# Optimization experiments

Hardware: AMD Instinct MI355X
Metric: run time of the kernel (lower is better)

Reference implementation:

```python
import jax, jax.numpy as jnp
import numpy as np

B, T, C, H, HS = 2, 2048, 1024, 16, 64
W_SIZE = 128
BLK = 64
NB = T // BLK            # 32 blocks
NSEL = 8                 # selected blocks per (b, h)
EPS = 1e-8


def setup_inputs() -> dict:
    key = jax.random.key(0)
    ks = jax.random.split(key, 12)
    s = 0.02
    return {
        "hidden_states": jax.random.normal(ks[0], (B, T, C), dtype=jnp.float32),
        "Wq": jax.random.normal(ks[1], (C, C), dtype=jnp.float32) * s,
        "bq": jnp.zeros((C,), jnp.float32),
        "Wk": jax.random.normal(ks[2], (C, C), dtype=jnp.float32) * s,
        "bk": jnp.zeros((C,), jnp.float32),
        "Wv": jax.random.normal(ks[3], (C, C), dtype=jnp.float32) * s,
        "bv": jnp.zeros((C,), jnp.float32),
        "Wo": jax.random.normal(ks[4], (C, C), dtype=jnp.float32) * s,
        "bo": jnp.zeros((C,), jnp.float32),
        "Wg": jax.random.normal(ks[5], (C, 3), dtype=jnp.float32) * s,
        "bg": jnp.zeros((3,), jnp.float32),
    }


def _sdpa(q, k, v, mask):
    # q: [B,H,Tq,HS], k/v: [B,H,S,HS], mask: [Tq,S] bool (True = attend)
    scale = 1.0 / jnp.sqrt(jnp.asarray(HS, q.dtype))
    scores = jnp.einsum('bhqd,bhkd->bhqk', q, k) * scale
    scores = jnp.where(mask, scores, jnp.asarray(-jnp.inf, scores.dtype))
    return jnp.einsum('bhqk,bhkd->bhqd', jax.nn.softmax(scores, axis=-1), v)


def _forward(x, Wq, bq, Wk, bk, Wv, bv, Wo, bo, Wg, bg):
    q = (x @ Wq + bq).reshape(B, T, H, HS).transpose(0, 2, 1, 3)
    k = (x @ Wk + bk).reshape(B, T, H, HS).transpose(0, 2, 1, 3)
    v = (x @ Wv + bv).reshape(B, T, H, HS).transpose(0, 2, 1, 3)

    gates = jax.nn.softmax(x @ Wg + bg, axis=-1)  # [B,T,3]
    g_sl, g_sel, g_cmp = gates[..., 0:1], gates[..., 1:2], gates[..., 2:3]

    i = jnp.arange(T)[:, None]

    # --- sliding-window branch (causal AND within window band) ---
    j = jnp.arange(T)[None, :]
    slide_mask = (j <= i) & (i - j <= W_SIZE)
    out_sl = _sdpa(q, k, v, slide_mask)

    # --- block representatives (mean-pooled K/V blocks) ---
    kb = k.reshape(B, H, NB, BLK, HS)
    vb = v.reshape(B, H, NB, BLK, HS)
    k_rep = kb.mean(axis=3)  # [B,H,NB,HS]

    # cosine similarity of each query vs each block rep, averaged over T
    qn = q / jnp.maximum(jnp.linalg.norm(q, axis=-1, keepdims=True), EPS)
    kn = k_rep / jnp.maximum(jnp.linalg.norm(k_rep, axis=-1, keepdims=True), EPS)
    global_scores = jnp.einsum('bhtd,bhnd->bhtn', qn, kn).mean(axis=2)  # [B,H,NB]
    _, top_idx = jax.lax.top_k(global_scores, NSEL)  # [B,H,NSEL]

    # gather selected K/V blocks
    sel_k = jnp.take_along_axis(kb, top_idx[..., None, None], axis=2).reshape(B, H, NSEL * BLK, HS)
    sel_v = jnp.take_along_axis(vb, top_idx[..., None, None], axis=2).reshape(B, H, NSEL * BLK, HS)

    # torch is_causal with Tq != S is top-left aligned: allow j <= i
    js = jnp.arange(NSEL * BLK)[None, :]
    out_sel = _sdpa(q, sel_k, sel_v, js <= i)

    # --- compressed branch over block reps ---
    v_cmp = vb.mean(axis=3)  # [B,H,NB,HS]
    jc = jnp.arange(NB)[None, :]
    out_cmp = _sdpa(q, k_rep, v_cmp, jc <= i)

    def merge(o):
        return o.transpose(0, 2, 1, 3).reshape(B, T, C)

    out = g_sl * merge(out_sl) + g_sel * merge(out_sel) + g_cmp * merge(out_cmp)
    return out @ Wo + bo


def reference(hidden_states, Wq, bq, Wk, bk, Wv, bv, Wo, bo, Wg, bg):
    return _forward(hidden_states, Wq, bq, Wk, bk, Wv, bv, Wo, bo, Wg, bg)
```

## Files before the change

kernel.cpp:

```cpp
#include <hip/hip_runtime.h>
#include <hip/hip_bf16.h>
#include <math.h>

#define Bc   2
#define Tc   2048
#define Cc   1024
#define Hc   16
#define HSc  64
#define WSZ  128
#define BLKc 64
#define NBc  32
#define NSELc 8
#define Mrows (Bc*Tc)
#define QCH  32
#define SOFT_C 4.0f

typedef __attribute__((ext_vector_type(8))) _Float16 half8;
typedef __attribute__((ext_vector_type(4))) float f32x4v;
typedef __attribute__((ext_vector_type(8))) unsigned short ushort8v;

__device__ __forceinline__ float wave_sum(float v) {
    #pragma unroll
    for (int o = 32; o; o >>= 1) v += __shfl_xor(v, o);
    return v;
}

__device__ __forceinline__ unsigned short f2h(float f) {
    _Float16 h = (_Float16)f;
    unsigned short u;
    __builtin_memcpy(&u, &h, 2);
    return u;
}
__device__ __forceinline__ float h2f(unsigned short u) {
    _Float16 h;
    __builtin_memcpy(&h, &u, 2);
    return (float)h;
}

__device__ __forceinline__ void gload16(const void* g, void* l) {
    __builtin_amdgcn_global_load_lds(
        (const __attribute__((address_space(1))) void*)g,
        (__attribute__((address_space(3))) void*)l, 16, 0, 0);
}

__global__ __launch_bounds__(256)
void cvt_front_kernel(const float* __restrict__ x, unsigned short* __restrict__ xb,
                      const float* __restrict__ Wg, const float* __restrict__ bg,
                      float* __restrict__ gates,
                      const float* __restrict__ W0, const float* __restrict__ W1,
                      const float* __restrict__ W2, const float* __restrict__ W3,
                      unsigned short* __restrict__ D012, unsigned short* __restrict__ D3)
{
    __shared__ float tile[64][65];
    const int bx = blockIdx.x;
    if (bx < 4096) {
        int i = (bx * 256 + threadIdx.x) * 4;
        float4 v = *(const float4*)&x[i];
        ushort4 o;
        o.x = f2h(v.x); o.y = f2h(v.y); o.z = f2h(v.z); o.w = f2h(v.w);
        *(ushort4*)&xb[i] = o;
        return;
    }
    if (bx < 5120) {
        const int row  = (bx - 4096) * 4 + (threadIdx.x >> 6);
        const int lane = threadIdx.x & 63;
        const float* xr = x + (size_t)row * Cc;
        float p0 = 0, p1 = 0, p2 = 0;
        #pragma unroll
        for (int it = 0; it < 4; ++it) {
            int k4 = lane * 4 + it * 256;
            float4 xv = *(const float4*)&xr[k4];
            float4 w0 = *(const float4*)&Wg[k4 * 3];
            float4 w1 = *(const float4*)&Wg[k4 * 3 + 4];
            float4 w2 = *(const float4*)&Wg[k4 * 3 + 8];
            p0 += xv.x * w0.x + xv.y * w0.w + xv.z * w1.z + xv.w * w2.y;
            p1 += xv.x * w0.y + xv.y * w1.x + xv.z * w1.w + xv.w * w2.z;
            p2 += xv.x * w0.z + xv.y * w1.y + xv.z * w2.x + xv.w * w2.w;
        }
        p0 = wave_sum(p0); p1 = wave_sum(p1); p2 = wave_sum(p2);
        if (lane == 0) {
            p0 += bg[0]; p1 += bg[1]; p2 += bg[2];
            float m = fmaxf(p0, fmaxf(p1, p2));
            float e0 = expf(p0 - m), e1 = expf(p1 - m), e2 = expf(p2 - m);
            float s = e0 + e1 + e2;
            gates[row * 3 + 0] = e0 / s;
            gates[row * 3 + 1] = e1 / s;
            gates[row * 3 + 2] = e2 / s;
        }
        return;
    }
    const int lin = bx - 5120;
    const int z = lin >> 8;
    const int n0 = (lin & 15) * 64, k0 = ((lin >> 4) & 15) * 64;
    const float* W = (z == 0) ? W0 : (z == 1) ? W1 : (z == 2) ? W2 : W3;
    unsigned short* WT = (z < 3) ? (D012 + (size_t)z * 1024 * 1024) : D3;
    const int tid = threadIdx.x;
    #pragma unroll
    for (int it = 0; it < 16; ++it) {
        int l2 = tid + it * 256;
        int r = l2 >> 6, c = l2 & 63;
        tile[r][c] = W[(size_t)(k0 + r) * 1024 + n0 + c];
    }
    __syncthreads();
    #pragma unroll
    for (int it = 0; it < 16; ++it) {
        int l2 = tid + it * 256;
        int n = l2 >> 6, k = l2 & 63;
        WT[(size_t)(n0 + n) * 1024 + k0 + k] = f2h(tile[k][n]);
    }
}


#define FENCE asm volatile("" ::: "memory")
#define BAR() do { FENCE; __builtin_amdgcn_s_barrier(); FENCE; } while(0)
#define WAIT_LGKM0() do { asm volatile("s_waitcnt lgkmcnt(0)" ::: "memory"); \
                          __builtin_amdgcn_sched_barrier(0); } while(0)
#define WAIT_VM(N) do { asm volatile("s_waitcnt vmcnt(" #N ")" ::: "memory"); } while(0)

#define LDA(BUF, MH) do { \
    const unsigned short* _p = &lds[BUF][0][(wmo + (MH)*64 + r16) * 64]; \
    a0[0] = *(const half8*)(_p +        cc0); a1[0] = *(const half8*)(_p +        cc1); \
    a0[1] = *(const half8*)(_p + 1024 + cc0); a1[1] = *(const half8*)(_p + 1024 + cc1); \
    a0[2] = *(const half8*)(_p + 2048 + cc0); a1[2] = *(const half8*)(_p + 2048 + cc1); \
    a0[3] = *(const half8*)(_p + 3072 + cc0); a1[3] = *(const half8*)(_p + 3072 + cc1); \
} while(0)

#define LDB(BUF, NH) do { \
    const unsigned short* _p = &lds[BUF][1][(wno + (NH)*32 + r16) * 64]; \
    b0[0] = *(const half8*)(_p +        cc0); b1[0] = *(const half8*)(_p +        cc1); \
    b0[1] = *(const half8*)(_p + 1024 + cc0); b1[1] = *(const half8*)(_p + 1024 + cc1); \
} while(0)

#define CLP(I, J, MH, NH) \
    acc[(MH)*4+(I)][(NH)*2+(J)] = __builtin_amdgcn_mfma_f32_16x16x32_f16(a0[I], b0[J], acc[(MH)*4+(I)][(NH)*2+(J)], 0, 0, 0); \
    acc[(MH)*4+(I)][(NH)*2+(J)] = __builtin_amdgcn_mfma_f32_16x16x32_f16(a1[I], b1[J], acc[(MH)*4+(I)][(NH)*2+(J)], 0, 0, 0);
#define CL(MH, NH) do { \
    __builtin_amdgcn_s_setprio(1); \
    CLP(0,0,MH,NH) CLP(0,1,MH,NH) CLP(1,0,MH,NH) CLP(1,1,MH,NH) \
    CLP(2,0,MH,NH) CLP(2,1,MH,NH) CLP(3,0,MH,NH) CLP(3,1,MH,NH) \
    __builtin_amdgcn_s_setprio(0); \
} while(0)

#define STAGEA(BUF, G, TILE) do { \
    size_t _co = (size_t)(TILE) * 64 + scol_x; \
    gload16(Ag + (size_t)(m0 +       (G)*64 + wid*8 + l8) * 1024 + _co, \
            &lds[BUF][0][((G)*64 + wid*8) * 64]); \
    gload16(Ag + (size_t)(m0 + 128 + (G)*64 + wid*8 + l8) * 1024 + _co, \
            &lds[BUF][0][(128 + (G)*64 + wid*8) * 64]); \
} while(0)

#define STAGEB(BUF, G, TILE) do { \
    size_t _co = (size_t)(TILE) * 64 + scol_x; \
    int _r0 = (wid >> 2) * 64 + (G)*32 + (wid & 3) * 8; \
    gload16(BTg + (size_t)(n0 +       _r0 + l8) * 1024 + _co, \
            &lds[BUF][1][_r0 * 64]); \
    gload16(BTg + (size_t)(n0 + 128 + _r0 + l8) * 1024 + _co, \
            &lds[BUF][1][(128 + _r0) * 64]); \
} while(0)

__global__ __launch_bounds__(512, 2)
void mfma_gemm_qkv8(const unsigned short* __restrict__ Ag,
                    const unsigned short* __restrict__ BTg,
                    const float* __restrict__ bq, const float* __restrict__ bk,
                    const float* __restrict__ bv,
                    unsigned short* __restrict__ Qh, unsigned short* __restrict__ Kf,
                    unsigned short* __restrict__ Vf)
{
    __shared__ unsigned short lds[2][2][256 * 64];
    const int tid  = threadIdx.x;
    const int lane = tid & 63, wid = tid >> 6;
    const int quad = lane >> 4, r16 = lane & 15;
    const int m0 = blockIdx.y * 256, n0 = blockIdx.x * 256;
    const int wmo = (wid >> 2) * 128;
    const int wno = (wid & 3) * 64;
    const int l8 = lane >> 3;
    const int scol_x = ((lane & 7) ^ l8) * 8;
    const int xsw = (r16 & 7) * 8;
    const int cc0 = (quad * 8) ^ xsw;
    const int cc1 = (32 + quad * 8) ^ xsw;

    f32x4v acc[8][4];
    #pragma unroll
    for (int i = 0; i < 8; ++i)
        #pragma unroll
        for (int j = 0; j < 4; ++j)
            acc[i][j] = (f32x4v){0.f, 0.f, 0.f, 0.f};

    half8 a0[4], a1[4], b0[2], b1[2];

    STAGEA(0, 0, 0); STAGEB(0, 1, 0); STAGEA(0, 1, 0); STAGEB(0, 0, 0);
    STAGEA(1, 0, 1); STAGEB(1, 1, 1);
    WAIT_VM(4);
    BAR();

    for (int it = 0; it < 8; ++it) {
        const int t1 = 2 * it + 1, t2v = 2 * it + 2, t3v = 2 * it + 3;
        const bool s2 = (t2v < 16), s3 = (t3v < 16);
        LDA(0, 0); LDB(0, 0);
        STAGEA(1, 1, t1);
        BAR(); WAIT_LGKM0();
        CL(0, 0);
        BAR();
        LDB(0, 1);
        STAGEB(1, 0, t1);
        BAR(); WAIT_LGKM0();
        CL(0, 1);
        BAR();
        LDA(0, 1);
        if (s2) STAGEA(0, 0, t2v);
        BAR(); WAIT_LGKM0();
        CL(1, 1);
        BAR();
        LDB(0, 0);
        if (s2) STAGEB(0, 1, t2v);
        BAR(); WAIT_LGKM0();
        CL(1, 0);
        if (it == 7) { WAIT_VM(0); } else { WAIT_VM(4); }
        BAR();
        LDA(1, 0); LDB(1, 0);
        if (s2) STAGEA(0, 1, t2v);
        BAR(); WAIT_LGKM0();
        CL(0, 0);
        BAR();
        LDB(1, 1);
        if (s2) STAGEB(0, 0, t2v);
        BAR(); WAIT_LGKM0();
        CL(0, 1);
        BAR();
        LDA(1, 1);
        if (s3) STAGEA(1, 0, t3v);
        BAR(); WAIT_LGKM0();
        CL(1, 1);
        BAR();
        LDB(1, 0);
        if (s3) STAGEB(1, 1, t3v);
        BAR(); WAIT_LGKM0();
        CL(1, 0);
        if (it < 7) WAIT_VM(4);
        BAR();
    }

    const int which = n0 >> 10;
    const float* bias = (which == 0) ? bq : ((which == 1) ? bk : bv);
    unsigned short* dst = (which == 0) ? Qh : ((which == 1) ? Kf : Vf);
    const float sc = (which == 0) ? 0.125f : 1.0f;
    #pragma unroll
    for (int i = 0; i < 8; ++i) {
        int mbase = m0 + wmo + i * 16 + quad * 4;
        #pragma unroll
        for (int j = 0; j < 4; ++j) {
            int n = n0 + wno + j * 16 + r16;
            int nn = n & 1023;
            float bvv = bias[nn];
            int h = nn >> 6, d = nn & 63;
            #pragma unroll
            for (int r = 0; r < 4; ++r) {
                int m = mbase + r;
                int b = m >> 11, t = m & 2047;
                float v = (acc[i][j][r] + bvv) * sc;
                dst[(((size_t)(b * Hc + h) * Tc) + t) * HSc + d] = f2h(v);
            }
        }
    }
}

#define OSTAGE(BUF, TILE) do { \
    size_t _t = (size_t)(TILE) * 64 + scol; \
    gload16(A  + (size_t)(m0 +      wid*8 + l8) * 1024 + _t, &As[BUF][( 0 + wid*64)*8]); \
    gload16(A  + (size_t)(m0 + 32 + wid*8 + l8) * 1024 + _t, &As[BUF][(256 + wid*64)*8]); \
    gload16(BT + (size_t)(n0 +      wid*8 + l8) * 1024 + _t, &Bs[BUF][( 0 + wid*64)*8]); \
    gload16(BT + (size_t)(n0 + 32 + wid*8 + l8) * 1024 + _t, &Bs[BUF][(256 + wid*64)*8]); \
    gload16(BT + (size_t)(n0 + 64 + wid*8 + l8) * 1024 + _t, &Bs[BUF][(512 + wid*64)*8]); \
    gload16(BT + (size_t)(n0 + 96 + wid*8 + l8) * 1024 + _t, &Bs[BUF][(768 + wid*64)*8]); \
} while(0)

__global__ __launch_bounds__(256, 2)
void mfma_gemm_oproj(const unsigned short* __restrict__ A,
                     const unsigned short* __restrict__ BT,
                     const float* __restrict__ bias,
                     float* __restrict__ Y)
{
    __shared__ unsigned short As[3][64 * 64];
    __shared__ unsigned short Bs[3][128 * 64];
    const int tid  = threadIdx.x;
    const int lane = tid & 63;
    const int wid  = tid >> 6;
    const int quad = lane >> 4, r16 = lane & 15;
    const int m0 = blockIdx.y * 64, n0 = blockIdx.x * 128;
    const int wm = (wid >> 1) * 32, wn = (wid & 1) * 64;
    const int l8 = lane >> 3;
    const int scol = ((lane & 7) ^ l8) * 8;
    const int xsw = (r16 & 7) * 8;
    const int cc0 = (quad * 8) ^ xsw;
    const int cc1 = (32 + quad * 8) ^ xsw;

    f32x4v acc[2][4];
    #pragma unroll
    for (int i = 0; i < 2; ++i)
        #pragma unroll
        for (int j = 0; j < 4; ++j)
            acc[i][j] = (f32x4v){0.f, 0.f, 0.f, 0.f};

    OSTAGE(0, 0); OSTAGE(1, 1);
    WAIT_VM(6);
    BAR();

    for (int t = 0; t < 16; ++t) {
        const int cb = t % 3;
        if (t + 2 < 16) OSTAGE((t + 2) % 3, t + 2);
        half8 af[2][2], bf[4][2];
        #pragma unroll
        for (int i = 0; i < 2; ++i) {
            const unsigned short* p = &As[cb][(wm + i * 16 + r16) * 64];
            af[i][0] = *(const half8*)(p + cc0);
            af[i][1] = *(const half8*)(p + cc1);
        }
        #pragma unroll
        for (int j = 0; j < 4; ++j) {
            const unsigned short* p = &Bs[cb][(wn + j * 16 + r16) * 64];
            bf[j][0] = *(const half8*)(p + cc0);
            bf[j][1] = *(const half8*)(p + cc1);
        }
        __builtin_amdgcn_s_setprio(1);
        #pragma unroll
        for (int i = 0; i < 2; ++i)
            #pragma unroll
            for (int j = 0; j < 4; ++j) {
                acc[i][j] = __builtin_amdgcn_mfma_f32_16x16x32_f16(af[i][0], bf[j][0], acc[i][j], 0, 0, 0);
                acc[i][j] = __builtin_amdgcn_mfma_f32_16x16x32_f16(af[i][1], bf[j][1], acc[i][j], 0, 0, 0);
            }
        __builtin_amdgcn_s_setprio(0);
        if (t + 2 < 16) { WAIT_VM(6); } else { WAIT_VM(0); }
        BAR();
    }

    #pragma unroll
    for (int i = 0; i < 2; ++i) {
        int mbase = m0 + wm + i * 16 + quad * 4;
        #pragma unroll
        for (int j = 0; j < 4; ++j) {
            int n = n0 + wn + j * 16 + r16;
            float bv = bias[n];
            #pragma unroll
            for (int r = 0; r < 4; ++r)
                Y[(size_t)(mbase + r) * 1024 + n] = acc[i][j][r] + bv;
        }
    }
}

__global__ __launch_bounds__(256)
void vtrans_stats_kernel(const unsigned short* __restrict__ Kf,
                         const unsigned short* __restrict__ Vf,
                         const unsigned short* __restrict__ Qh,
                         unsigned short* __restrict__ Vt,
                         float* __restrict__ krep,
                         unsigned short* __restrict__ krep16,
                         unsigned short* __restrict__ vcmpT16,
                         float* __restrict__ qpart)
{
    __shared__ unsigned short vtile[64][65];
    __shared__ unsigned short ktile[64][65];
    __shared__ float rinv[64];
    const int nb = blockIdx.x, bh = blockIdx.y;
    const int t0 = nb * BLKc;
    const int tid = threadIdx.x;
    const int c4 = (tid & 15) * 4, r = tid >> 4;
    const unsigned short* vsrc = Vf + ((size_t)bh * Tc + t0) * HSc;
    const unsigned short* ksrc = Kf + ((size_t)bh * Tc + t0) * HSc;
    #pragma unroll
    for (int it = 0; it < 4; ++it) {
        int tt = r + it * 16;
        *(ushort4*)&vtile[tt][c4] = *(const ushort4*)&vsrc[(size_t)tt * HSc + c4];
        *(ushort4*)&ktile[tt][c4] = *(const ushort4*)&ksrc[(size_t)tt * HSc + c4];
    }
    __syncthreads();
    unsigned short* dst = Vt + (size_t)bh * HSc * Tc + t0;
    #pragma unroll
    for (int it = 0; it < 4; ++it) {
        int d = r + it * 16;
        ushort4 o;
        o.x = vtile[c4 + 0][d]; o.y = vtile[c4 + 1][d];
        o.z = vtile[c4 + 2][d]; o.w = vtile[c4 + 3][d];
        *(ushort4*)&dst[(size_t)d * Tc + c4] = o;
    }
    const int wid = tid >> 6, lane = tid & 63;
    if (wid == 0) {
        const int d = lane;
        float sk = 0.f, sv = 0.f;
        #pragma unroll 8
        for (int t = 0; t < BLKc; ++t) {
            sk += h2f(ktile[t][d]);
            sv += h2f(vtile[t][d]);
        }
        float km = sk * (1.0f / BLKc), vm = sv * (1.0f / BLKc);
        krep[((size_t)bh * NBc + nb) * HSc + d] = km;
        krep16[(size_t)bh * 4096 + nb * 64 + d] = f2h(km);
        krep16[(size_t)bh * 4096 + (nb + 32) * 64 + d] = 0;
        vcmpT16[(size_t)bh * 4096 + d * 64 + nb] = f2h(vm);
        vcmpT16[(size_t)bh * 4096 + d * 64 + nb + 32] = 0;
    } else if (wid == 1) {
        const unsigned short* qbase = Qh + ((size_t)bh * Tc + t0) * HSc;
        {
            const unsigned short* qr = qbase + (size_t)lane * HSc;
            float ss = 0.f;
            #pragma unroll
            for (int d8 = 0; d8 < 8; ++d8) {
                ushort8v v8 = *(const ushort8v*)&qr[d8 * 8];
                #pragma unroll
                for (int j = 0; j < 8; ++j) { float f = h2f(v8[j]); ss += f * f; }
            }
            rinv[lane] = 1.0f / fmaxf(sqrtf(ss), 1e-8f);
        }
        float acc = 0.f;
        #pragma unroll 8
        for (int t = 0; t < 64; ++t)
            acc += h2f(qbase[(size_t)t * HSc + lane]) * rinv[t];
        qpart[((size_t)bh * QCH + nb) * HSc + lane] = acc;
    }
}

__global__ __launch_bounds__(64)
void topk_kernel(const float* __restrict__ qpart, const float* __restrict__ krep,
                 int* __restrict__ topidx)
{
    int bh = blockIdx.x, lane = threadIdx.x;
    __shared__ float sc[NBc];
    __shared__ float qbs[HSc];
    float qa = 0.0f;
    #pragma unroll
    for (int c = 0; c < QCH; c++)
        qa += qpart[((size_t)bh * QCH + c) * HSc + lane];
    qbs[lane] = qa * (1.0f / Tc);
    __syncthreads();
    if (lane < NBc) {
        float dot = 0, nk = 0;
        for (int d = 0; d < HSc; d++) {
            float kv = krep[((size_t)bh * NBc + lane) * HSc + d];
            nk += kv * kv;
            dot += qbs[d] * kv;
        }
        sc[lane] = dot / fmaxf(sqrtf(nk), 1e-8f);
    }
    __syncthreads();
    if (lane == 0) {
        for (int s = 0; s < NSELc; s++) {
            int best = 0; float bv = sc[0];
            for (int n = 1; n < NBc; n++)
                if (sc[n] > bv) { bv = sc[n]; best = n; }
            topidx[bh * NSELc + s] = best;
            sc[best] = -INFINITY;
        }
    }
}

__device__ __forceinline__ void fa_desc(int i, int nslide, int nsel, int q0,
                                        const int* __restrict__ topidx, int bh,
                                        int& kb, int& p0v, int& wl, int& kl, int& bid)
{
    if (i < nslide)             { kb = q0 - (nslide - 1 - i) * 64;
                                  p0v = kb; wl = WSZ; kl = 64; bid = 0; }
    else if (i < nslide + nsel) { int s = i - nslide;
                                  kb = topidx[bh * NSELc + s] * BLKc;
                                  p0v = s * BLKc; wl = 1 << 30; kl = 64; bid = 1; }
    else                        { kb = 0; p0v = 0; wl = 1 << 30; kl = NBc; bid = 2; }
}

__device__ __forceinline__ void fa_ldtile(int kb, int bid,
                                          const unsigned short* __restrict__ kbh,
                                          const unsigned short* __restrict__ vbh,
                                          const unsigned short* __restrict__ krepb,
                                          const unsigned short* __restrict__ vcmpb,
                                          int r0, int seg,
                                          ushort8v& k0, ushort8v& k1,
                                          ushort8v& v0, ushort8v& v1)
{
    const unsigned short *kp, *vp;
    int vs;
    if (bid < 2) { kp = kbh + (size_t)kb * HSc; vp = vbh + kb; vs = Tc; }
    else         { kp = krepb; vp = vcmpb; vs = 64; }
    k0 = *(const ushort8v*)(kp + (size_t)r0 * HSc + seg * 8);
    k1 = *(const ushort8v*)(kp + (size_t)(r0 + 32) * HSc + seg * 8);
    v0 = *(const ushort8v*)(vp + (size_t)r0 * vs + seg * 8);
    v1 = *(const ushort8v*)(vp + (size_t)(r0 + 32) * vs + seg * 8);
}

__device__ __forceinline__ void fa_qkt(const unsigned short* __restrict__ Kh,
                                       half8 aq0, half8 aq1, int l16, int kc0, int kc1,
                                       f32x4v s[4])
{
    #pragma unroll
    for (int t = 0; t < 4; ++t) {
        f32x4v sa = (f32x4v){0.f, 0.f, 0.f, 0.f};
        half8 b0 = *(const half8*)&Kh[(t * 16 + l16) * 64 + kc0];
        half8 b1 = *(const half8*)&Kh[(t * 16 + l16) * 64 + kc1];
        sa = __builtin_amdgcn_mfma_f32_16x16x32_f16(aq0, b0, sa, 0, 0, 0);
        sa = __builtin_amdgcn_mfma_f32_16x16x32_f16(aq1, b1, sa, 0, 0, 0);
        s[t] = sa;
    }
}

__device__ __forceinline__ void fa_expph(const f32x4v s[4], int p0v, int wl, int kl,
                                         int qg0, int prow, int l16,
                                         unsigned short* __restrict__ Ph)
{
    #pragma unroll
    for (int t = 0; t < 4; ++t) {
        int kk = t * 16 + l16;
        bool kok = kk < kl;
        int jt = p0v + kk;
        #pragma unroll
        for (int r = 0; r < 4; ++r) {
            bool valid = kok && ((unsigned)(qg0 + r - jt) <= (unsigned)wl);
            float p = valid ? __expf(s[t][r] - SOFT_C) : 0.0f;
            int row = prow + r;
            Ph[row * 64 + (kk ^ ((row & 7) * 8))] = f2h(p);
        }
    }
}

__device__ __forceinline__ void fa_pv(const unsigned short* __restrict__ Vt,
                                      const unsigned short* __restrict__ Ph,
                                      half8 ones, int wq, int l16, int kc0, int kc1,
                                      f32x4v o[4], f32x4v& o5)
{
    const int prd = (wq + l16) * 64;
    half8 ap0 = *(const half8*)&Ph[prd + kc0];
    half8 ap1 = *(const half8*)&Ph[prd + kc1];
    o5 = __builtin_amdgcn_mfma_f32_16x16x32_f16(ap0, ones, o5, 0, 0, 0);
    o5 = __builtin_amdgcn_mfma_f32_16x16x32_f16(ap1, ones, o5, 0, 0, 0);
    #pragma unroll
    for (int dt = 0; dt < 4; ++dt) {
        half8 v0 = *(const half8*)&Vt[(dt * 16 + l16) * 64 + kc0];
        half8 v1 = *(const half8*)&Vt[(dt * 16 + l16) * 64 + kc1];
        o[dt] = __builtin_amdgcn_mfma_f32_16x16x32_f16(ap0, v0, o[dt], 0, 0, 0);
        o[dt] = __builtin_amdgcn_mfma_f32_16x16x32_f16(ap1, v1, o[dt], 0, 0, 0);
    }
}

__global__ __launch_bounds__(256, 2)
void fattn_kernel(const unsigned short* __restrict__ Qh16,
                  const unsigned short* __restrict__ Kf,
                  const unsigned short* __restrict__ Vtg,
                  const unsigned short* __restrict__ krep16,
                  const unsigned short* __restrict__ vcmpT16,
                  const int* __restrict__ topidx,
                  const float* __restrict__ gates, unsigned short* __restrict__ merged)
{
    __shared__ unsigned short KH[2][64 * 64];
    __shared__ unsigned short VT[2][64 * 64];
    __shared__ unsigned short Ph[64 * 64];

    const int qt = blockIdx.x;
    const int bh = blockIdx.y;
    const int b  = bh >> 4, h = bh & 15;
    const int tid  = threadIdx.x;
    const int wid  = tid >> 6, lane = tid & 63;
    const int l16  = lane & 15, quad = lane >> 4;
    const int q0 = qt * 64;
    const int wq = wid * 16;
    const int qg0 = q0 + wq + quad * 4;
    const int prow = wq + quad * 4;

    const int nslide = (qt < 2 ? qt : 2) + 1;
    const int nsel   = (qt + 1 < NSELc) ? (qt + 1) : NSELc;
    const int nt     = nslide + nsel + 1;

    half8 aq0, aq1, ones;
    {
        const unsigned short* qrow = Qh16 + ((size_t)bh * Tc + q0 + wq + l16) * HSc;
        aq0 = *(const half8*)(qrow + quad * 8);
        aq1 = *(const half8*)(qrow + 32 + quad * 8);
        #pragma unroll
        for (int j = 0; j < 8; ++j) ones[j] = (_Float16)1.0f;
    }

    f32x4v o[4], macc[4];
    f32x4v o5 = (f32x4v){0.f, 0.f, 0.f, 0.f};
    #pragma unroll
    for (int dt = 0; dt < 4; ++dt) {
        o[dt]    = (f32x4v){0.f, 0.f, 0.f, 0.f};
        macc[dt] = (f32x4v){0.f, 0.f, 0.f, 0.f};
    }

    const int seg = tid & 7, r0 = tid >> 3;
    const int stc = (seg ^ (r0 & 7)) * 8;
    const int st0 = r0 * 64 + stc;
    const int st1 = (r0 + 32) * 64 + stc;
    const int psw = (l16 & 7) * 8;
    const int kc0 = (quad * 8) ^ psw;
    const int kc1 = (32 + quad * 8) ^ psw;

    const unsigned short* kbh  = Kf  + (size_t)bh * Tc * HSc;
    const unsigned short* vbh  = Vtg + (size_t)bh * HSc * Tc;
    const unsigned short* krepb = krep16  + (size_t)bh * 4096;
    const unsigned short* vcmpb = vcmpT16 + (size_t)bh * 4096;

#define FA_MERGE(PB) do { \
    _Pragma("unroll") \
    for (int r = 0; r < 4; ++r) { \
        float g = gates[((size_t)b * Tc + qg0 + r) * 3 + (PB)]; \
        float inv = g / o5[r]; \
        _Pragma("unroll") \
        for (int dt = 0; dt < 4; ++dt) { macc[dt][r] += inv * o[dt][r]; o[dt][r] = 0.f; } \
        o5[r] = 0.f; \
    } \
} while(0)

    {
        int kb, p0v, wl, kl, bid;
        ushort8v k0, k1, v0, v1;
        fa_desc(0, nslide, nsel, q0, topidx, bh, kb, p0v, wl, kl, bid);
        fa_ldtile(kb, bid, kbh, vbh, krepb, vcmpb, r0, seg, k0, k1, v0, v1);
        *(ushort8v*)&KH[0][st0] = k0; *(ushort8v*)&KH[0][st1] = k1;
        *(ushort8v*)&VT[0][st0] = v0; *(ushort8v*)&VT[0][st1] = v1;
        fa_desc(1, nslide, nsel, q0, topidx, bh, kb, p0v, wl, kl, bid);
        fa_ldtile(kb, bid, kbh, vbh, krepb, vcmpb, r0, seg, k0, k1, v0, v1);
        *(ushort8v*)&KH[1][st0] = k0; *(ushort8v*)&KH[1][st1] = k1;
        *(ushort8v*)&VT[1][st0] = v0; *(ushort8v*)&VT[1][st1] = v1;
    }
    __syncthreads();

    int pb = 0;
    for (int i = 0; i < nt; i += 2) {
        const bool dual = (i + 1 < nt);
        const bool pf2  = (i + 2 < nt);
        const bool pf3  = (i + 3 < nt);

        ushort8v pk0[2], pk1[2], pv0[2], pv1[2];
        if (pf2) {
            int kb, p0v, wl, kl, bid;
            fa_desc(i + 2, nslide, nsel, q0, topidx, bh, kb, p0v, wl, kl, bid);
            fa_ldtile(kb, bid, kbh, vbh, krepb, vcmpb, r0, seg,
                      pk0[0], pk1[0], pv0[0], pv1[0]);
        }
        if (pf3) {
            int kb, p0v, wl, kl, bid;
            fa_desc(i + 3, nslide, nsel, q0, topidx, bh, kb, p0v, wl, kl, bid);
            fa_ldtile(kb, bid, kbh, vbh, krepb, vcmpb, r0, seg,
                      pk0[1], pk1[1], pv0[1], pv1[1]);
        }

        int kbA, p0A, wlA, klA, bidA;
        fa_desc(i, nslide, nsel, q0, topidx, bh, kbA, p0A, wlA, klA, bidA);
        int kbB, p0B, wlB, klB, bidB = bidA;
        if (dual) fa_desc(i + 1, nslide, nsel, q0, topidx, bh, kbB, p0B, wlB, klB, bidB);

        f32x4v sA[4], sB[4];
        fa_qkt(KH[0], aq0, aq1, l16, kc0, kc1, sA);
        if (dual) fa_qkt(KH[1], aq0, aq1, l16, kc0, kc1, sB);

        if (bidA != pb) { FA_MERGE(pb); pb = bidA; }
        fa_expph(sA, p0A, wlA, klA, qg0, prow, l16, Ph);
        fa_pv(VT[0], Ph, ones, wq, l16, kc0, kc1, o, o5);

        if (dual) {
            if (bidB != pb) { FA_MERGE(pb); pb = bidB; }
            fa_expph(sB, p0B, wlB, klB, qg0, prow, l16, Ph);
            fa_pv(VT[1], Ph, ones, wq, l16, kc0, kc1, o, o5);
        }

        if (pf2) {
            __syncthreads();
            *(ushort8v*)&KH[0][st0] = pk0[0]; *(ushort8v*)&KH[0][st1] = pk1[0];
            *(ushort8v*)&VT[0][st0] = pv0[0]; *(ushort8v*)&VT[0][st1] = pv1[0];
            if (pf3) {
                *(ushort8v*)&KH[1][st0] = pk0[1]; *(ushort8v*)&KH[1][st1] = pk1[1];
                *(ushort8v*)&VT[1][st0] = pv0[1]; *(ushort8v*)&VT[1][st1] = pv1[1];
            }
            __syncthreads();
        }
    }

    #pragma unroll
    for (int r = 0; r < 4; ++r) {
        float g = gates[((size_t)b * Tc + qg0 + r) * 3 + 2];
        float inv = g / o5[r];
        #pragma unroll
        for (int dt = 0; dt < 4; ++dt) macc[dt][r] += inv * o[dt][r];
    }

    #pragma unroll
    for (int r = 0; r < 4; ++r) {
        size_t mrow = (size_t)b * Tc + qg0 + r;
        #pragma unroll
        for (int dt = 0; dt < 4; ++dt)
            merged[mrow * Cc + h * HSc + dt * 16 + l16] = f2h(macc[dt][r]);
    }
#undef FA_MERGE
}

extern "C" void kernel_launch(void* const* d_in, const int* in_sizes, int n_in,
                              void* d_out, int out_size, void* d_ws, size_t ws_size,
                              hipStream_t stream)
{
    const float* x  = (const float*)d_in[0];
    const float* Wq = (const float*)d_in[1];
    const float* bq = (const float*)d_in[2];
    const float* Wk = (const float*)d_in[3];
    const float* bk = (const float*)d_in[4];
    const float* Wv = (const float*)d_in[5];
    const float* bv = (const float*)d_in[6];
    const float* Wo = (const float*)d_in[7];
    const float* bo = (const float*)d_in[8];
    const float* Wg = (const float*)d_in[9];
    const float* bg = (const float*)d_in[10];
    float* out = (float*)d_out;
    float* ws  = (float*)d_ws;

    unsigned short* Qh16 = (unsigned short*)(ws + 0);
    unsigned short* Kf16 = (unsigned short*)(ws + 2097152);
    unsigned short* Vf16 = (unsigned short*)(ws + 4194304);
    unsigned short* Vt16 = (unsigned short*)(ws + 6291456);
    unsigned short* Mgb  = (unsigned short*)(ws + 8388608);
    unsigned short* xb   = (unsigned short*)(ws + 10485760);
    unsigned short* WqkvT = (unsigned short*)(ws + 12582912);
    unsigned short* WoT   = (unsigned short*)(ws + 14155776);
    float* gates = ws + 14680064;
    float* krep  = ws + 14692352;
    unsigned short* krep16  = (unsigned short*)(ws + 14757888);
    unsigned short* vcmpT16 = (unsigned short*)(ws + 14823424);
    float* qpart = ws + 14888960;
    int*   topidx = (int*)(ws + 14954496);

    cvt_front_kernel<<<6144, 256, 0, stream>>>(x, xb, Wg, bg, gates,
                                               Wq, Wk, Wv, Wo, WqkvT, WoT);

    mfma_gemm_qkv8<<<dim3(12, 16), 512, 0, stream>>>(xb, WqkvT, bq, bk, bv,
                                                     Qh16, Kf16, Vf16);
    vtrans_stats_kernel<<<dim3(NBc, Bc * Hc), 256, 0, stream>>>(Kf16, Vf16, Qh16,
                                                                Vt16, krep, krep16,
                                                                vcmpT16, qpart);
    topk_kernel<<<Bc * Hc, 64, 0, stream>>>(qpart, krep, topidx);
    fattn_kernel<<<dim3(Tc / 64, Bc * Hc), 256, 0, stream>>>(Qh16, Kf16, Vt16,
                                                             krep16, vcmpT16,
                                                             topidx, gates, Mgb);
    mfma_gemm_oproj<<<dim3(8, 64), 256, 0, stream>>>(Mgb, WoT, bo, out);
}
```

Measured before the change: 201.4 us.

## Software-pipeline attention loop with 4-slot K/V ring and double-buffered P

Replaces the two-tiles-per-iteration loop with a one-tile-per-iteration software pipeline. The QK^T and exp of tile i now run alongside the PV product of tile i-1, using a 4-deep shared K/V ring buffer and double-buffered probability tiles. The aim is to cut barriers from two per tile pair to one per tile and to overlap MFMA work across stages. In exchange, shared memory per block roughly doubles, which could limit occupancy, and the merge ordering now depends on the deferred PV.

```diff
diff --git a/kernel.cpp b/kernel.cpp
--- a/kernel.cpp
+++ b/kernel.cpp
@@ -546,9 +546,9 @@
                   const int* __restrict__ topidx,
                   const float* __restrict__ gates, unsigned short* __restrict__ merged)
 {
-    __shared__ unsigned short KH[2][64 * 64];
-    __shared__ unsigned short VT[2][64 * 64];
-    __shared__ unsigned short Ph[64 * 64];
+    __shared__ unsigned short KH[4][64 * 64];
+    __shared__ unsigned short VT[4][64 * 64];
+    __shared__ unsigned short Ph[2][64 * 64];
 
     const int qt = blockIdx.x;
     const int bh = blockIdx.y;
@@ -620,57 +620,39 @@
     }
     __syncthreads();
 
-    int pb = 0;
-    for (int i = 0; i < nt; i += 2) {
-        const bool dual = (i + 1 < nt);
-        const bool pf2  = (i + 2 < nt);
-        const bool pf3  = (i + 3 < nt);
-
-        ushort8v pk0[2], pk1[2], pv0[2], pv1[2];
-        if (pf2) {
+    int pbid = 0;
+    for (int i = 0; i < nt; ++i) {
+        const bool pf = (i + 2 < nt);
+        ushort8v k0, k1, v0, v1;
+        if (pf) {
             int kb, p0v, wl, kl, bid;
             fa_desc(i + 2, nslide, nsel, q0, topidx, bh, kb, p0v, wl, kl, bid);
-            fa_ldtile(kb, bid, kbh, vbh, krepb, vcmpb, r0, seg,
-                      pk0[0], pk1[0], pv0[0], pv1[0]);
-        }
-        if (pf3) {
-            int kb, p0v, wl, kl, bid;
-            fa_desc(i + 3, nslide, nsel, q0, topidx, bh, kb, p0v, wl, kl, bid);
-            fa_ldtile(kb, bid, kbh, vbh, krepb, vcmpb, r0, seg,
-                      pk0[1], pk1[1], pv0[1], pv1[1]);
-        }
-
-        int kbA, p0A, wlA, klA, bidA;
-        fa_desc(i, nslide, nsel, q0, topidx, bh, kbA, p0A, wlA, klA, bidA);
-        int kbB, p0B, wlB, klB, bidB = bidA;
-        if (dual) fa_desc(i + 1, nslide, nsel, q0, topidx, bh, kbB, p0B, wlB, klB, bidB);
-
-        f32x4v sA[4], sB[4];
-        fa_qkt(KH[0], aq0, aq1, l16, kc0, kc1, sA);
-        if (dual) fa_qkt(KH[1], aq0, aq1, l16, kc0, kc1, sB);
-
-        if (bidA != pb) { FA_MERGE(pb); pb = bidA; }
-        fa_expph(sA, p0A, wlA, klA, qg0, prow, l16, Ph);
-        fa_pv(VT[0], Ph, ones, wq, l16, kc0, kc1, o, o5);
-
-        if (dual) {
-            if (bidB != pb) { FA_MERGE(pb); pb = bidB; }
-            fa_expph(sB, p0B, wlB, klB, qg0, prow, l16, Ph);
-            fa_pv(VT[1], Ph, ones, wq, l16, kc0, kc1, o, o5);
-        }
-
-        if (pf2) {
+            fa_ldtile(kb, bid, kbh, vbh, krepb, vcmpb, r0, seg, k0, k1, v0, v1);
+        }
+        int kb, p0v, wl, kl, bid;
+        fa_desc(i, nslide, nsel, q0, topidx, bh, kb, p0v, wl, kl, bid);
+
+        f32x4v s[4];
+        fa_qkt(KH[i & 3], aq0, aq1, l16, kc0, kc1, s);
+
+        if (i > 0) {
+            fa_pv(VT[(i - 1) & 3], Ph[(i - 1) & 1], ones, wq, l16, kc0, kc1, o, o5);
+            if (bid != pbid) { FA_MERGE(pbid); }
+        }
+        pbid = bid;
+
+        fa_expph(s, p0v, wl, kl, qg0, prow, l16, Ph[i & 1]);
+
+        if (pf) {
+            *(ushort8v*)&KH[(i + 2) & 3][st0] = k0;
+            *(ushort8v*)&KH[(i + 2) & 3][st1] = k1;
+            *(ushort8v*)&VT[(i + 2) & 3][st0] = v0;
+            *(ushort8v*)&VT[(i + 2) & 3][st1] = v1;
             __syncthreads();
-            *(ushort8v*)&KH[0][st0] = pk0[0]; *(ushort8v*)&KH[0][st1] = pk1[0];
-            *(ushort8v*)&VT[0][st0] = pv0[0]; *(ushort8v*)&VT[0][st1] = pv1[0];
-            if (pf3) {
-                *(ushort8v*)&KH[1][st0] = pk0[1]; *(ushort8v*)&KH[1][st1] = pk1[1];
-                *(ushort8v*)&VT[1][st0] = pv0[1]; *(ushort8v*)&VT[1][st1] = pv1[1];
-            }
-            __syncthreads();
-        }
-    }
-
+        }
+    }
+
+    fa_pv(VT[(nt - 1) & 3], Ph[(nt - 1) & 1], ones, wq, l16, kc0, kc1, o, o5);
     #pragma unroll
     for (int r = 0; r < 4; ++r) {
         float g = gates[((size_t)b * Tc + qg0 + r) * 3 + 2];
```

Measured after the change: 203.2 us. No clear change (+0.9%).
